# Performance work log

Hardware: AMD Instinct MI355X
Metric: run time of the kernel (lower is better)

Reference implementation:

```python
import jax, jax.numpy as jnp
import numpy as np

N_WAY, N_SHOT, C, H, W = 5, 5, 640, 32, 32
EPS = 1e-12


def conv1x1(x, w, b):
    # 1x1 conv == channel GEMM; w: (C_out, C_in), b: (C_out,)
    return jnp.einsum('bchw,oc->bohw', x, w) + b[None, :, None, None]


def setup_inputs() -> dict:
    key = jax.random.key(0)
    ks = jax.random.split(key, 7)
    B = N_WAY * N_SHOT
    x5 = jax.random.normal(ks[0], (B, C, H, W), jnp.float32)
    Wc = jax.random.normal(ks[1], (C, C), jnp.float32) * 0.02
    bc = jax.random.normal(ks[2], (C,), jnp.float32) * 0.02
    Wq = jax.random.normal(ks[3], (C, C), jnp.float32) * 0.02
    bq = jax.random.normal(ks[4], (C,), jnp.float32) * 0.02
    Wk = jax.random.normal(ks[5], (C, C), jnp.float32) * 0.02
    bk = jax.random.normal(ks[6], (C,), jnp.float32) * 0.02
    return {"x5": x5, "Wc": Wc, "bc": bc, "Wq": Wq, "bq": bq, "Wk": Wk, "bk": bk}


def reference(x5, Wc, bc, Wq, bq, Wk, bk):
    B, Cc, Hh, Ww = x5.shape
    HW = Hh * Ww
    scale = 1.0 / (Cc ** 0.5)

    # residual 1x1 conv, then query_transform applied once (x5 is reassigned)
    x5 = conv1x1(x5, Wc, bc) + x5
    x5 = conv1x1(x5, Wq, bq)

    # query: query_transform applied AGAIN on the already-transformed x5
    xq = conv1x1(x5, Wq, bq).reshape(N_WAY, N_SHOT, Cc, HW)
    xq = xq.transpose(0, 1, 3, 2).reshape(N_WAY, N_SHOT * HW, Cc)
    xk = conv1x1(x5, Wk, bk).reshape(N_WAY, N_SHOT, Cc, HW)
    xk = xk.transpose(0, 2, 1, 3).reshape(N_WAY, Cc, N_SHOT * HW)

    # QK scores per way: (n_way, S*HW, S*HW)
    xw = jnp.matmul(xq, xk) * scale
    # max over key spatial, mean over key shot
    xw = xw.reshape(N_WAY, N_SHOT * HW, N_SHOT, HW).max(-1).mean(-1)
    xw = jax.nn.softmax(xw.reshape(N_WAY, N_SHOT, HW), axis=-1)

    # channel-wise L2 normalize (F.normalize semantics)
    nrm = jnp.maximum(jnp.sqrt((x5 * x5).sum(1, keepdims=True)), EPS)
    norm0 = (x5 / nrm).reshape(N_WAY, N_SHOT, Cc, Hh, Ww)

    # argmax-equality mask over spatial positions
    xw_max = xw.max(-1, keepdims=True)
    mask = (xw == xw_max).astype(x5.dtype).reshape(N_WAY, N_SHOT, 1, Hh, Ww)

    # seeds: masked spatial sum of normalized features -> (n_way, n_shot, C)
    seeds = (norm0 * mask).sum((3, 4))

    # conv3d correlation: out[b,o,h,w] = sum_{k,c} norm0[b,k,c,h,w] * seeds[o,k,c]
    cm = jnp.einsum('bkchw,okc->bohw', norm0, seeds).reshape(N_WAY, N_WAY, HW)
    cmin = cm.min(-1, keepdims=True)
    cmax = cm.max(-1, keepdims=True)
    cm = (cm - cmin) / (cmax - cmin + EPS)
    cormap = cm.reshape(B, 1, Hh, Ww)

    x51 = (x5 * cormap).reshape(N_WAY, N_SHOT, Cc, Hh, Ww)
    proto1 = x51.mean((1, 3, 4))  # (n_way, C)
    return proto1
```

## Files before the change

kernel.cpp:

```cpp
#include <hip/hip_runtime.h>
#include <math.h>

#define NW 5
#define NS 5
#define CDIM 640
#define HWDIM 1024
#define BDIM 25
constexpr int CHW = CDIM * HWDIM;
constexpr int NBIG = BDIM * CHW;
constexpr int WSZ = CDIM * CDIM;
constexpr float QK_SCALE = 0.03952847075210474f;

typedef __attribute__((ext_vector_type(4))) float f32x4;
typedef __attribute__((ext_vector_type(8))) __bf16 bf16x8;
typedef __attribute__((ext_vector_type(4))) __bf16 bf16x4;
typedef __attribute__((ext_vector_type(2))) __bf16 bf16x2;

__device__ __forceinline__ void load_lds16(const __bf16* g, __bf16* l) {
    __builtin_amdgcn_global_load_lds(
        (const __attribute__((address_space(1))) void*)g,
        (__attribute__((address_space(3))) void*)l, 16, 0, 0);
}

__global__ __launch_bounds__(256) void split_f32(const float* __restrict__ s,
                                                 __bf16* __restrict__ dH,
                                                 __bf16* __restrict__ dL, int n4) {
    int i = blockIdx.x * 256 + threadIdx.x;
    if (i >= n4) return;
    f32x4 v = reinterpret_cast<const f32x4*>(s)[i];
    bf16x4 h, lo;
    #pragma unroll
    for (int q = 0; q < 4; ++q) {
        __bf16 hh = (__bf16)v[q];
        h[q] = hh;
        lo[q] = (__bf16)(v[q] - (float)hh);
    }
    reinterpret_cast<bf16x4*>(dH)[i] = h;
    reinterpret_cast<bf16x4*>(dL)[i] = lo;
}

__global__ __launch_bounds__(256) void tsplit(const float* __restrict__ x,
                                              __bf16* __restrict__ dH,
                                              __bf16* __restrict__ dL) {
    __shared__ float sT[32][33];
    const int hw0 = blockIdx.x * 32, c0 = blockIdx.y * 32, b = blockIdx.z;
    const int t = threadIdx.x;
    const int r = t >> 3, q4 = (t & 7) * 4;
    f32x4 v = *reinterpret_cast<const f32x4*>(
        &x[(size_t)b * CHW + (size_t)(c0 + r) * HWDIM + hw0 + q4]);
    #pragma unroll
    for (int i = 0; i < 4; ++i) sT[r][q4 + i] = v[i];
    __syncthreads();
    bf16x4 h, lo;
    #pragma unroll
    for (int i = 0; i < 4; ++i) {
        float xv = sT[q4 + i][r];
        __bf16 hh = (__bf16)xv;
        h[i] = hh;
        lo[i] = (__bf16)(xv - (float)hh);
    }
    size_t off = (size_t)b * CHW + (size_t)(hw0 + r) * CDIM + c0 + q4;
    *reinterpret_cast<bf16x4*>(&dH[off]) = h;
    *reinterpret_cast<bf16x4*>(&dL[off]) = lo;
}


__device__ __forceinline__ void stage_tile(const __bf16* __restrict__ srcH,
                                           const __bf16* __restrict__ srcL,
                                           __bf16* lds, int wv, int l, int c0) {
    const int lch = (l & 7) ^ (l >> 3);
    const int scol = (lch & 3) * 8;
    const int srw = l >> 3;
    const __bf16* src = (lch & 4) ? srcL : srcH;
    #pragma unroll
    for (int i = 0; i < 4; ++i) {
        const int r0 = wv * 32 + i * 8;
        load_lds16(&src[(size_t)(r0 + srw) * CDIM + c0 + scol], &lds[r0 * 64]);
    }
}

template <int RES>
__global__ __launch_bounds__(256) void conv_mfma(
    const __bf16* __restrict__ inH, const __bf16* __restrict__ inL,
    const __bf16* __restrict__ wH, const __bf16* __restrict__ wL,
    const float* __restrict__ bias,
    __bf16* __restrict__ outH, __bf16* __restrict__ outL) {
    __shared__ __bf16 sA[128 * 64];
    __shared__ __bf16 sB[128 * 64];
    const int hw0 = blockIdx.x * 128;
    const int o0 = blockIdx.y * 128;
    const int b = blockIdx.z;
    const int tid = threadIdx.x;
    const int wv = tid >> 6, l = tid & 63;
    const int wo = (wv >> 1) * 64, wh = (wv & 1) * 64;
    const size_t inBase = (size_t)b * CHW;

    const __bf16* wSrcH = wH + (size_t)o0 * CDIM;
    const __bf16* wSrcL = wL + (size_t)o0 * CDIM;
    const __bf16* iSrcH = inH + inBase + (size_t)hw0 * CDIM;
    const __bf16* iSrcL = inL + inBase + (size_t)hw0 * CDIM;

    f32x4 acc[4][4];
    #pragma unroll
    for (int i = 0; i < 4; ++i)
        #pragma unroll
        for (int j = 0; j < 4; ++j) acc[i][j] = (f32x4){0.f, 0.f, 0.f, 0.f};

    const int fr = l & 15, cf = l >> 4;
    const int ehi = (cf ^ (fr & 7)) * 8;

    for (int c0 = 0; c0 < CDIM; c0 += 32) {
        stage_tile(wSrcH, wSrcL, sA, wv, l, c0);
        stage_tile(iSrcH, iSrcL, sB, wv, l, c0);
        __syncthreads();
        bf16x8 aH[4], aL[4], bH[4], bL[4];
        #pragma unroll
        for (int i = 0; i < 4; ++i) {
            const int ra = (wo + i * 16 + fr) * 64;
            const int rb = (wh + i * 16 + fr) * 64;
            aH[i] = *reinterpret_cast<const bf16x8*>(&sA[ra + ehi]);
            aL[i] = *reinterpret_cast<const bf16x8*>(&sA[ra + (ehi ^ 32)]);
            bH[i] = *reinterpret_cast<const bf16x8*>(&sB[rb + ehi]);
            bL[i] = *reinterpret_cast<const bf16x8*>(&sB[rb + (ehi ^ 32)]);
        }
        #pragma unroll
        for (int i = 0; i < 4; ++i)
            #pragma unroll
            for (int j = 0; j < 4; ++j) {
                acc[i][j] = __builtin_amdgcn_mfma_f32_16x16x32_bf16(
                    aH[i], bH[j], acc[i][j], 0, 0, 0);
                acc[i][j] = __builtin_amdgcn_mfma_f32_16x16x32_bf16(
                    aH[i], bL[j], acc[i][j], 0, 0, 0);
                acc[i][j] = __builtin_amdgcn_mfma_f32_16x16x32_bf16(
                    aL[i], bH[j], acc[i][j], 0, 0, 0);
            }
        __syncthreads();
    }

    const int og = (l >> 4) * 4;
    const int cl = l & 15;
    #pragma unroll
    for (int i = 0; i < 4; ++i) {
        const int o = o0 + wo + i * 16 + og;
        const f32x4 bs = *reinterpret_cast<const f32x4*>(&bias[o]);
        #pragma unroll
        for (int j = 0; j < 4; ++j) {
            const int hw = hw0 + wh + j * 16 + cl;
            const size_t off = inBase + (size_t)hw * CDIM + o;
            float r[4];
            #pragma unroll
            for (int q = 0; q < 4; ++q) r[q] = acc[i][j][q] + bs[q];
            if (RES) {
                bf16x4 rh = *reinterpret_cast<const bf16x4*>(&inH[off]);
                bf16x4 rl = *reinterpret_cast<const bf16x4*>(&inL[off]);
                #pragma unroll
                for (int q = 0; q < 4; ++q) r[q] += (float)rh[q] + (float)rl[q];
            }
            bf16x4 oh, ol;
            #pragma unroll
            for (int q = 0; q < 4; ++q) {
                __bf16 hh = (__bf16)r[q];
                oh[q] = hh;
                ol[q] = (__bf16)(r[q] - (float)hh);
            }
            *reinterpret_cast<bf16x4*>(&outH[off]) = oh;
            *reinterpret_cast<bf16x4*>(&outL[off]) = ol;
        }
    }
}

__global__ __launch_bounds__(256) void attn_mfma(
    const __bf16* __restrict__ qH, const __bf16* __restrict__ qL,
    const __bf16* __restrict__ kH, const __bf16* __restrict__ kL,
    float* __restrict__ gpart) {
    __shared__ __bf16 sQ[128 * 64];
    __shared__ __bf16 sK[128 * 64];
    __shared__ float sRed[2][128];
    const int qt = blockIdx.x;
    const int ks = blockIdx.y, wy = blockIdx.z;
    const int sq = qt >> 3, q0 = (qt & 7) * 128;
    const int tid = threadIdx.x;
    const int wv = tid >> 6, l = tid & 63;
    const int wq = (wv >> 1) * 64;
    const int kh = wv & 1;
    const int wk = kh * 64;
    const __bf16* qSrcH = qH + (size_t)(wy * NS + sq) * CHW + (size_t)q0 * CDIM;
    const __bf16* qSrcL = qL + (size_t)(wy * NS + sq) * CHW + (size_t)q0 * CDIM;
    const __bf16* kBaseH = kH + (size_t)(wy * NS + ks) * CHW;
    const __bf16* kBaseL = kL + (size_t)(wy * NS + ks) * CHW;

    float qmax[4][4];
    #pragma unroll
    for (int i = 0; i < 4; ++i)
        #pragma unroll
        for (int q = 0; q < 4; ++q) qmax[i][q] = -INFINITY;

    const int fr = l & 15, cf = l >> 4;
    const int ehi = (cf ^ (fr & 7)) * 8;

    for (int kc = 0; kc < HWDIM; kc += 128) {
        const __bf16* kSrcH = kBaseH + (size_t)kc * CDIM;
        const __bf16* kSrcL = kBaseL + (size_t)kc * CDIM;
        f32x4 acc[4][4];
        #pragma unroll
        for (int i = 0; i < 4; ++i)
            #pragma unroll
            for (int j = 0; j < 4; ++j) acc[i][j] = (f32x4){0.f, 0.f, 0.f, 0.f};

        for (int c0 = 0; c0 < CDIM; c0 += 32) {
            stage_tile(qSrcH, qSrcL, sQ, wv, l, c0);
            stage_tile(kSrcH, kSrcL, sK, wv, l, c0);
            __syncthreads();
            bf16x8 aH[4], aL[4], bH[4], bL[4];
            #pragma unroll
            for (int i = 0; i < 4; ++i) {
                const int ra = (wq + i * 16 + fr) * 64;
                const int rb = (wk + i * 16 + fr) * 64;
                aH[i] = *reinterpret_cast<const bf16x8*>(&sQ[ra + ehi]);
                aL[i] = *reinterpret_cast<const bf16x8*>(&sQ[ra + (ehi ^ 32)]);
                bH[i] = *reinterpret_cast<const bf16x8*>(&sK[rb + ehi]);
                bL[i] = *reinterpret_cast<const bf16x8*>(&sK[rb + (ehi ^ 32)]);
            }
            __builtin_amdgcn_s_setprio(1);
            #pragma unroll
            for (int i = 0; i < 4; ++i)
                #pragma unroll
                for (int j = 0; j < 4; ++j) {
                    acc[i][j] = __builtin_amdgcn_mfma_f32_16x16x32_bf16(
                        aH[i], bH[j], acc[i][j], 0, 0, 0);
                    acc[i][j] = __builtin_amdgcn_mfma_f32_16x16x32_bf16(
                        aH[i], bL[j], acc[i][j], 0, 0, 0);
                    acc[i][j] = __builtin_amdgcn_mfma_f32_16x16x32_bf16(
                        aL[i], bH[j], acc[i][j], 0, 0, 0);
                }
            __builtin_amdgcn_s_setprio(0);
            __syncthreads();
        }
        #pragma unroll
        for (int i = 0; i < 4; ++i)
            #pragma unroll
            for (int q = 0; q < 4; ++q) {
                float m = fmaxf(fmaxf(acc[i][0][q], acc[i][1][q]),
                                fmaxf(acc[i][2][q], acc[i][3][q]));
                qmax[i][q] = fmaxf(qmax[i][q], m);
            }
    }
    #pragma unroll
    for (int i = 0; i < 4; ++i)
        #pragma unroll
        for (int q = 0; q < 4; ++q) {
            float v = qmax[i][q];
            v = fmaxf(v, __shfl_xor(v, 1));
            v = fmaxf(v, __shfl_xor(v, 2));
            v = fmaxf(v, __shfl_xor(v, 4));
            v = fmaxf(v, __shfl_xor(v, 8));
            qmax[i][q] = v;
        }
    if ((l & 15) == 0) {
        const int g = l >> 4;
        #pragma unroll
        for (int i = 0; i < 4; ++i)
            #pragma unroll
            for (int q = 0; q < 4; ++q)
                sRed[kh][wq + i * 16 + g * 4 + q] = qmax[i][q];
    }
    __syncthreads();
    if (tid < 128) {
        float m = fmaxf(sRed[0][tid], sRed[1][tid]);
        gpart[(size_t)(wy * NS + ks) * (NS * HWDIM) + sq * HWDIM + q0 + tid] =
            m * QK_SCALE;
    }
}

__global__ __launch_bounds__(256) void softmax_mask(const float* __restrict__ gpart,
                                                    int* __restrict__ gIdx,
                                                    int* __restrict__ gCnt) {
    const int bb = blockIdx.x;
    const int w = bb / NS, sq = bb % NS;
    const int tid = threadIdx.x;
    __shared__ float sred[256];
    __shared__ int sCnt;

    float v[4];
    #pragma unroll
    for (int i = 0; i < 4; ++i) {
        int hw = tid + 256 * i;
        float s = 0.f;
        #pragma unroll
        for (int ks = 0; ks < NS; ++ks)
            s += gpart[(size_t)(w * NS + ks) * (NS * HWDIM) + sq * HWDIM + hw];
        v[i] = s * 0.2f;
    }
    float m = fmaxf(fmaxf(v[0], v[1]), fmaxf(v[2], v[3]));
    sred[tid] = m;
    __syncthreads();
    for (int s = 128; s > 0; s >>= 1) {
        if (tid < s) sred[tid] = fmaxf(sred[tid], sred[tid + s]);
        __syncthreads();
    }
    float rowmax = sred[0];
    __syncthreads();
    float e[4], ls = 0.f;
    #pragma unroll
    for (int i = 0; i < 4; ++i) { e[i] = expf(v[i] - rowmax); ls += e[i]; }
    sred[tid] = ls;
    __syncthreads();
    for (int s = 128; s > 0; s >>= 1) {
        if (tid < s) sred[tid] += sred[tid + s];
        __syncthreads();
    }
    float ssum = sred[0];
    __syncthreads();
    float p[4], pm = 0.f;
    #pragma unroll
    for (int i = 0; i < 4; ++i) { p[i] = e[i] / ssum; pm = fmaxf(pm, p[i]); }
    sred[tid] = pm;
    __syncthreads();
    for (int s = 128; s > 0; s >>= 1) {
        if (tid < s) sred[tid] = fmaxf(sred[tid], sred[tid + s]);
        __syncthreads();
    }
    float pmax = sred[0];
    if (tid == 0) sCnt = 0;
    __syncthreads();
    #pragma unroll
    for (int i = 0; i < 4; ++i) {
        if (p[i] == pmax) {
            int slot = atomicAdd(&sCnt, 1);
            gIdx[bb * HWDIM + slot] = tid + 256 * i;
        }
    }
    __syncthreads();
    if (tid == 0) gCnt[bb] = sCnt;
}

__global__ __launch_bounds__(256) void nrm_k(const __bf16* __restrict__ yH,
                                             const __bf16* __restrict__ yL,
                                             float* __restrict__ inv) {
    const int row = blockIdx.x * 16 + (threadIdx.x >> 4);
    const int cq = threadIdx.x & 15;
    const size_t base = (size_t)row * CDIM;
    float s = 0.f;
    #pragma unroll
    for (int i = 0; i < 10; ++i) {
        int c = i * 64 + cq * 4;
        bf16x4 h = *reinterpret_cast<const bf16x4*>(&yH[base + c]);
        bf16x4 lo = *reinterpret_cast<const bf16x4*>(&yL[base + c]);
        #pragma unroll
        for (int q = 0; q < 4; ++q) {
            float x = (float)h[q] + (float)lo[q];
            s = fmaf(x, x, s);
        }
    }
    s += __shfl_xor(s, 1);
    s += __shfl_xor(s, 2);
    s += __shfl_xor(s, 4);
    s += __shfl_xor(s, 8);
    if (cq == 0) inv[row] = 1.0f / fmaxf(sqrtf(s), 1e-12f);
}

__global__ __launch_bounds__(640) void seeds_k(const __bf16* __restrict__ yH,
                                               const __bf16* __restrict__ yL,
                                               const float* __restrict__ inv,
                                               const int* __restrict__ gIdx,
                                               const int* __restrict__ gCnt,
                                               float* __restrict__ seeds) {
    const int bb = blockIdx.x, c = threadIdx.x;
    const int cnt = gCnt[bb];
    float s = 0.f;
    for (int e = 0; e < cnt; ++e) {
        int hw = gIdx[bb * HWDIM + e];
        size_t off = (size_t)bb * CHW + (size_t)hw * CDIM + c;
        s += ((float)yH[off] + (float)yL[off]) * inv[bb * HWDIM + hw];
    }
    seeds[bb * CDIM + c] = s;
}

__global__ __launch_bounds__(256) void cm_k(const __bf16* __restrict__ yH,
                                            const __bf16* __restrict__ yL,
                                            const float* __restrict__ inv,
                                            const float* __restrict__ seeds,
                                            float* __restrict__ cm) {
    __shared__ float sS[BDIM * CDIM];
    const int way = blockIdx.y;
    const int tid = threadIdx.x, wv = tid >> 6, l = tid & 63;
    const int hw = blockIdx.x * 4 + wv;
    for (int e = tid; e < BDIM * CDIM; e += 256) sS[e] = seeds[e];
    __syncthreads();
    float acc[NW] = {0.f, 0.f, 0.f, 0.f, 0.f};
    for (int k = 0; k < NS; ++k) {
        const size_t base = (size_t)(way * NS + k) * CHW + (size_t)hw * CDIM;
        float t[NW] = {0.f, 0.f, 0.f, 0.f, 0.f};
        #pragma unroll
        for (int i = 0; i < 5; ++i) {
            int c = (i * 64 + l) * 2;
            bf16x2 h = *reinterpret_cast<const bf16x2*>(&yH[base + c]);
            bf16x2 lo = *reinterpret_cast<const bf16x2*>(&yL[base + c]);
            float x0 = (float)h[0] + (float)lo[0];
            float x1 = (float)h[1] + (float)lo[1];
            #pragma unroll
            for (int o = 0; o < NW; ++o) {
                t[o] = fmaf(x0, sS[(o * NS + k) * CDIM + c], t[o]);
                t[o] = fmaf(x1, sS[(o * NS + k) * CDIM + c + 1], t[o]);
            }
        }
        float iv = inv[(way * NS + k) * HWDIM + hw];
        #pragma unroll
        for (int o = 0; o < NW; ++o) acc[o] = fmaf(t[o], iv, acc[o]);
    }
    #pragma unroll
    for (int o = 0; o < NW; ++o) {
        float v = acc[o];
        v += __shfl_xor(v, 1);
        v += __shfl_xor(v, 2);
        v += __shfl_xor(v, 4);
        v += __shfl_xor(v, 8);
        v += __shfl_xor(v, 16);
        v += __shfl_xor(v, 32);
        if (l == 0) cm[(size_t)(way * NW + o) * HWDIM + hw] = v;
    }
}

__global__ __launch_bounds__(256) void minmax_kernel(float* __restrict__ cm) {
    const int row = blockIdx.x;
    const int tid = threadIdx.x;
    __shared__ float smn[256], smx[256];
    float v[4];
    #pragma unroll
    for (int i = 0; i < 4; ++i) v[i] = cm[(size_t)row * HWDIM + tid + 256 * i];
    float mn = fminf(fminf(v[0], v[1]), fminf(v[2], v[3]));
    float mx = fmaxf(fmaxf(v[0], v[1]), fmaxf(v[2], v[3]));
    smn[tid] = mn;
    smx[tid] = mx;
    __syncthreads();
    for (int s = 128; s > 0; s >>= 1) {
        if (tid < s) {
            smn[tid] = fminf(smn[tid], smn[tid + s]);
            smx[tid] = fmaxf(smx[tid], smx[tid + s]);
        }
        __syncthreads();
    }
    float cmin = smn[0], cmax = smx[0];
    float den = cmax - cmin + 1e-12f;
    #pragma unroll
    for (int i = 0; i < 4; ++i)
        cm[(size_t)row * HWDIM + tid + 256 * i] = (v[i] - cmin) / den;
}

__global__ __launch_bounds__(128) void proto_part_k(const __bf16* __restrict__ yH,
                                                    const __bf16* __restrict__ yL,
                                                    const float* __restrict__ cmn,
                                                    float* __restrict__ part) {
    const int w = blockIdx.x, cc = blockIdx.y, hs = blockIdx.z;
    const int c = cc * 128 + threadIdx.x;
    float s = 0.f;
    for (int i = 0; i < 640; ++i) {
        int g = hs * 640 + i, sh = g >> 10, hw = g & 1023;
        size_t off = (size_t)(w * NS + sh) * CHW + (size_t)hw * CDIM + c;
        s = fmaf((float)yH[off] + (float)yL[off],
                 cmn[(w * NS + sh) * HWDIM + hw], s);
    }
    part[((w * 5 + cc) * 8 + hs) * 128 + threadIdx.x] = s;
}

__global__ __launch_bounds__(128) void proto_red_k(const float* __restrict__ part,
                                                   float* __restrict__ out) {
    const int bid = blockIdx.x;
    float s = 0.f;
    #pragma unroll
    for (int hs = 0; hs < 8; ++hs) s += part[(bid * 8 + hs) * 128 + threadIdx.x];
    const int w = bid / 5, cc = bid % 5;
    out[w * CDIM + cc * 128 + threadIdx.x] = s * (1.0f / 5120.0f);
}

extern "C" void kernel_launch(void* const* d_in, const int* in_sizes, int n_in,
                              void* d_out, int out_size, void* d_ws, size_t ws_size,
                              hipStream_t stream) {
    const float* x5 = (const float*)d_in[0];
    const float* Wc = (const float*)d_in[1];
    const float* bc = (const float*)d_in[2];
    const float* Wq = (const float*)d_in[3];
    const float* bq = (const float*)d_in[4];
    const float* Wk = (const float*)d_in[5];
    const float* bk = (const float*)d_in[6];
    float* out = (float*)d_out;

    __bf16* big = (__bf16*)d_ws;
    __bf16* A_hi = big;
    __bf16* A_lo = big + (size_t)NBIG;
    __bf16* B_hi = big + (size_t)2 * NBIG;
    __bf16* B_lo = big + (size_t)3 * NBIG;
    __bf16* C_hi = big + (size_t)4 * NBIG;
    __bf16* C_lo = big + (size_t)5 * NBIG;
    __bf16* wp = big + (size_t)6 * NBIG;
    __bf16* WcH = wp;
    __bf16* WcL = wp + WSZ;
    __bf16* WqH = wp + 2 * WSZ;
    __bf16* WqL = wp + 3 * WSZ;
    __bf16* WkH = wp + 4 * WSZ;
    __bf16* WkL = wp + 5 * WSZ;
    float* fp = (float*)(wp + 6 * WSZ);
    float* gpart = fp;
    float* invb = fp + 128000;
    float* seedsb = fp + 153600;
    float* cmb = fp + 169600;
    float* partb = fp + 195200;
    int* gIdx = (int*)(fp + 220800);
    int* gCnt = gIdx + BDIM * HWDIM;

    const int W4 = WSZ / 4;
    split_f32<<<dim3((W4 + 255) / 256), 256, 0, stream>>>(Wc, WcH, WcL, W4);
    split_f32<<<dim3((W4 + 255) / 256), 256, 0, stream>>>(Wq, WqH, WqL, W4);
    split_f32<<<dim3((W4 + 255) / 256), 256, 0, stream>>>(Wk, WkH, WkL, W4);
    tsplit<<<dim3(32, 20, 25), 256, 0, stream>>>(x5, A_hi, A_lo);

    dim3 gG(8, 5, 25);
    conv_mfma<1><<<gG, 256, 0, stream>>>(A_hi, A_lo, WcH, WcL, bc, B_hi, B_lo);
    conv_mfma<0><<<gG, 256, 0, stream>>>(B_hi, B_lo, WqH, WqL, bq, C_hi, C_lo);
    conv_mfma<0><<<gG, 256, 0, stream>>>(C_hi, C_lo, WqH, WqL, bq, B_hi, B_lo);
    conv_mfma<0><<<gG, 256, 0, stream>>>(C_hi, C_lo, WkH, WkL, bk, A_hi, A_lo);

    attn_mfma<<<dim3(40, 5, 5), 256, 0, stream>>>(B_hi, B_lo, A_hi, A_lo, gpart);
    softmax_mask<<<25, 256, 0, stream>>>(gpart, gIdx, gCnt);
    nrm_k<<<1600, 256, 0, stream>>>(C_hi, C_lo, invb);
    seeds_k<<<25, 640, 0, stream>>>(C_hi, C_lo, invb, gIdx, gCnt, seedsb);
    cm_k<<<dim3(256, 5), 256, 0, stream>>>(C_hi, C_lo, invb, seedsb, cmb);
    minmax_kernel<<<25, 256, 0, stream>>>(cmb);
    proto_part_k<<<dim3(5, 5, 8), 128, 0, stream>>>(C_hi, C_lo, cmb, partb);
    proto_red_k<<<25, 128, 0, stream>>>(partb, out);
}
```

Before: 1.084 ms.

## Double-buffer LDS tiles in conv and attention MFMA kernels

Both the conv and attention MFMA kernels now use two LDS buffers per operand. The next K-slice is prefetched with global_load_lds while MFMAs run on the current buffer, so global load latency overlaps compute instead of stalling before each step. In the attention kernel the prefetch runs continuously across key-chunk boundaries. LDS per block doubles, which may cut occupancy, and correctness depends on the trailing syncthreads covering the async loads.

```diff
diff --git a/kernel.cpp b/kernel.cpp
--- a/kernel.cpp
+++ b/kernel.cpp
@@ -64,7 +64,6 @@
     *reinterpret_cast<bf16x4*>(&dL[off]) = lo;
 }
 
-
 __device__ __forceinline__ void stage_tile(const __bf16* __restrict__ srcH,
                                            const __bf16* __restrict__ srcL,
                                            __bf16* lds, int wv, int l, int c0) {
@@ -85,8 +84,8 @@
     const __bf16* __restrict__ wH, const __bf16* __restrict__ wL,
     const float* __restrict__ bias,
     __bf16* __restrict__ outH, __bf16* __restrict__ outL) {
-    __shared__ __bf16 sA[128 * 64];
-    __shared__ __bf16 sB[128 * 64];
+    __shared__ __bf16 sA[2][128 * 64];
+    __shared__ __bf16 sB[2][128 * 64];
     const int hw0 = blockIdx.x * 128;
     const int o0 = blockIdx.y * 128;
     const int b = blockIdx.z;
@@ -109,19 +108,26 @@
     const int fr = l & 15, cf = l >> 4;
     const int ehi = (cf ^ (fr & 7)) * 8;
 
-    for (int c0 = 0; c0 < CDIM; c0 += 32) {
-        stage_tile(wSrcH, wSrcL, sA, wv, l, c0);
-        stage_tile(iSrcH, iSrcL, sB, wv, l, c0);
-        __syncthreads();
+    stage_tile(wSrcH, wSrcL, sA[0], wv, l, 0);
+    stage_tile(iSrcH, iSrcL, sB[0], wv, l, 0);
+    __syncthreads();
+
+    constexpr int NT = CDIM / 32;
+    for (int t = 0; t < NT; ++t) {
+        const int cur = t & 1;
+        if (t + 1 < NT) {
+            stage_tile(wSrcH, wSrcL, sA[cur ^ 1], wv, l, (t + 1) * 32);
+            stage_tile(iSrcH, iSrcL, sB[cur ^ 1], wv, l, (t + 1) * 32);
+        }
         bf16x8 aH[4], aL[4], bH[4], bL[4];
         #pragma unroll
         for (int i = 0; i < 4; ++i) {
             const int ra = (wo + i * 16 + fr) * 64;
             const int rb = (wh + i * 16 + fr) * 64;
-            aH[i] = *reinterpret_cast<const bf16x8*>(&sA[ra + ehi]);
-            aL[i] = *reinterpret_cast<const bf16x8*>(&sA[ra + (ehi ^ 32)]);
-            bH[i] = *reinterpret_cast<const bf16x8*>(&sB[rb + ehi]);
-            bL[i] = *reinterpret_cast<const bf16x8*>(&sB[rb + (ehi ^ 32)]);
+            aH[i] = *reinterpret_cast<const bf16x8*>(&sA[cur][ra + ehi]);
+            aL[i] = *reinterpret_cast<const bf16x8*>(&sA[cur][ra + (ehi ^ 32)]);
+            bH[i] = *reinterpret_cast<const bf16x8*>(&sB[cur][rb + ehi]);
+            bL[i] = *reinterpret_cast<const bf16x8*>(&sB[cur][rb + (ehi ^ 32)]);
         }
         #pragma unroll
         for (int i = 0; i < 4; ++i)
@@ -173,8 +179,8 @@
     const __bf16* __restrict__ qH, const __bf16* __restrict__ qL,
     const __bf16* __restrict__ kH, const __bf16* __restrict__ kL,
     float* __restrict__ gpart) {
-    __shared__ __bf16 sQ[128 * 64];
-    __shared__ __bf16 sK[128 * 64];
+    __shared__ __bf16 sQ[2][128 * 64];
+    __shared__ __bf16 sK[2][128 * 64];
     __shared__ float sRed[2][128];
     const int qt = blockIdx.x;
     const int ks = blockIdx.y, wy = blockIdx.z;
@@ -198,28 +204,39 @@
     const int fr = l & 15, cf = l >> 4;
     const int ehi = (cf ^ (fr & 7)) * 8;
 
-    for (int kc = 0; kc < HWDIM; kc += 128) {
-        const __bf16* kSrcH = kBaseH + (size_t)kc * CDIM;
-        const __bf16* kSrcL = kBaseL + (size_t)kc * CDIM;
+    constexpr int NC = CDIM / 32;
+
+    stage_tile(qSrcH, qSrcL, sQ[0], wv, l, 0);
+    stage_tile(kBaseH, kBaseL, sK[0], wv, l, 0);
+    __syncthreads();
+
+    for (int kci = 0; kci < 8; ++kci) {
         f32x4 acc[4][4];
         #pragma unroll
         for (int i = 0; i < 4; ++i)
             #pragma unroll
             for (int j = 0; j < 4; ++j) acc[i][j] = (f32x4){0.f, 0.f, 0.f, 0.f};
 
-        for (int c0 = 0; c0 < CDIM; c0 += 32) {
-            stage_tile(qSrcH, qSrcL, sQ, wv, l, c0);
-            stage_tile(kSrcH, kSrcL, sK, wv, l, c0);
-            __syncthreads();
+        for (int ci = 0; ci < NC; ++ci) {
+            const int step = kci * NC + ci;
+            const int cur = step & 1;
+            int nc = ci + 1, nkc = kci;
+            if (nc == NC) { nc = 0; ++nkc; }
+            if (nkc < 8) {
+                stage_tile(qSrcH, qSrcL, sQ[cur ^ 1], wv, l, nc * 32);
+                stage_tile(kBaseH + (size_t)(nkc * 128) * CDIM,
+                           kBaseL + (size_t)(nkc * 128) * CDIM,
+                           sK[cur ^ 1], wv, l, nc * 32);
+            }
             bf16x8 aH[4], aL[4], bH[4], bL[4];
             #pragma unroll
             for (int i = 0; i < 4; ++i) {
                 const int ra = (wq + i * 16 + fr) * 64;
                 const int rb = (wk + i * 16 + fr) * 64;
-                aH[i] = *reinterpret_cast<const bf16x8*>(&sQ[ra + ehi]);
-                aL[i] = *reinterpret_cast<const bf16x8*>(&sQ[ra + (ehi ^ 32)]);
-                bH[i] = *reinterpret_cast<const bf16x8*>(&sK[rb + ehi]);
-                bL[i] = *reinterpret_cast<const bf16x8*>(&sK[rb + (ehi ^ 32)]);
+                aH[i] = *reinterpret_cast<const bf16x8*>(&sQ[cur][ra + ehi]);
+                aL[i] = *reinterpret_cast<const bf16x8*>(&sQ[cur][ra + (ehi ^ 32)]);
+                bH[i] = *reinterpret_cast<const bf16x8*>(&sK[cur][rb + ehi]);
+                bL[i] = *reinterpret_cast<const bf16x8*>(&sK[cur][rb + (ehi ^ 32)]);
             }
             __builtin_amdgcn_s_setprio(1);
             #pragma unroll
```

Result: no change. 1.082 ms (-0.2%).

## Fold residual conv into Wq, fuse Q/K convs, widen GEMM tiles

Applied to the files above, without the earlier changes.

The residual 1x1 conv followed by the Wq conv is rewritten algebraically as a single GEMM with W2 = Wq·(Wc+I) and bias Wq·bc+bq, both precomputed on device. This removes one full-size conv pass. The two convs that read the same input (Wq and Wk) now run in a single launch with a concatenated bias. Both the conv and attention kernels move to 128x256 tiles to get more reuse per LDS load. In exchange, the weights are rounded differently in the combined product, and the larger accumulator arrays raise register pressure.

```diff
diff --git a/kernel.cpp b/kernel.cpp
--- a/kernel.cpp
+++ b/kernel.cpp
@@ -64,8 +64,43 @@
     *reinterpret_cast<bf16x4*>(&dL[off]) = lo;
 }
 
-
-__device__ __forceinline__ void stage_tile(const __bf16* __restrict__ srcH,
+__global__ __launch_bounds__(256) void wtsplit(const float* __restrict__ W,
+                                               __bf16* __restrict__ dH,
+                                               __bf16* __restrict__ dL) {
+    __shared__ float sT[32][33];
+    const int ci0 = blockIdx.x * 32, t0 = blockIdx.y * 32;
+    const int t = threadIdx.x;
+    const int r = t >> 3, q4 = (t & 7) * 4;
+    f32x4 v = *reinterpret_cast<const f32x4*>(&W[(size_t)(t0 + r) * CDIM + ci0 + q4]);
+    #pragma unroll
+    for (int i = 0; i < 4; ++i) sT[r][q4 + i] = v[i];
+    __syncthreads();
+    bf16x4 h, lo;
+    #pragma unroll
+    for (int i = 0; i < 4; ++i) {
+        float xv = sT[q4 + i][r];
+        if (t0 + q4 + i == ci0 + r) xv += 1.0f;
+        __bf16 hh = (__bf16)xv;
+        h[i] = hh;
+        lo[i] = (__bf16)(xv - (float)hh);
+    }
+    size_t off = (size_t)(ci0 + r) * CDIM + t0 + q4;
+    *reinterpret_cast<bf16x4*>(&dH[off]) = h;
+    *reinterpret_cast<bf16x4*>(&dL[off]) = lo;
+}
+
+__global__ void zero_k(float* __restrict__ p) { p[threadIdx.x] = 0.0f; }
+
+__global__ void bias1_k(const float* __restrict__ Wq, const float* __restrict__ bc,
+                        const float* __restrict__ bq, float* __restrict__ B2) {
+    const int o = threadIdx.x;
+    float s = bq[o];
+    for (int t = 0; t < CDIM; ++t) s = fmaf(Wq[(size_t)o * CDIM + t], bc[t], s);
+    B2[o] = s;
+}
+
+template <int NL>
+__device__ __forceinline__ void stage_rows(const __bf16* __restrict__ srcH,
                                            const __bf16* __restrict__ srcL,
                                            __bf16* lds, int wv, int l, int c0) {
     const int lch = (l & 7) ^ (l >> 3);
@@ -73,14 +108,13 @@
     const int srw = l >> 3;
     const __bf16* src = (lch & 4) ? srcL : srcH;
     #pragma unroll
-    for (int i = 0; i < 4; ++i) {
-        const int r0 = wv * 32 + i * 8;
+    for (int i = 0; i < NL; ++i) {
+        const int r0 = wv * (8 * NL) + i * 8;
         load_lds16(&src[(size_t)(r0 + srw) * CDIM + c0 + scol], &lds[r0 * 64]);
     }
 }
 
-template <int RES>
-__global__ __launch_bounds__(256) void conv_mfma(
+__global__ __launch_bounds__(256) void gemm_sm(
     const __bf16* __restrict__ inH, const __bf16* __restrict__ inL,
     const __bf16* __restrict__ wH, const __bf16* __restrict__ wL,
     const float* __restrict__ bias,
@@ -89,16 +123,14 @@
     __shared__ __bf16 sB[128 * 64];
     const int hw0 = blockIdx.x * 128;
     const int o0 = blockIdx.y * 128;
-    const int b = blockIdx.z;
     const int tid = threadIdx.x;
     const int wv = tid >> 6, l = tid & 63;
     const int wo = (wv >> 1) * 64, wh = (wv & 1) * 64;
-    const size_t inBase = (size_t)b * CHW;
 
     const __bf16* wSrcH = wH + (size_t)o0 * CDIM;
     const __bf16* wSrcL = wL + (size_t)o0 * CDIM;
-    const __bf16* iSrcH = inH + inBase + (size_t)hw0 * CDIM;
-    const __bf16* iSrcL = inL + inBase + (size_t)hw0 * CDIM;
+    const __bf16* iSrcH = inH + (size_t)hw0 * CDIM;
+    const __bf16* iSrcL = inL + (size_t)hw0 * CDIM;
 
     f32x4 acc[4][4];
     #pragma unroll
@@ -110,8 +142,8 @@
     const int ehi = (cf ^ (fr & 7)) * 8;
 
     for (int c0 = 0; c0 < CDIM; c0 += 32) {
-        stage_tile(wSrcH, wSrcL, sA, wv, l, c0);
-        stage_tile(iSrcH, iSrcL, sB, wv, l, c0);
+        stage_rows<4>(wSrcH, wSrcL, sA, wv, l, c0);
+        stage_rows<4>(iSrcH, iSrcL, sB, wv, l, c0);
         __syncthreads();
         bf16x8 aH[4], aL[4], bH[4], bL[4];
         #pragma unroll
@@ -146,22 +178,14 @@
         #pragma unroll
         for (int j = 0; j < 4; ++j) {
             const int hw = hw0 + wh + j * 16 + cl;
-            const size_t off = inBase + (size_t)hw * CDIM + o;
-            float r[4];
-            #pragma unroll
-            for (int q = 0; q < 4; ++q) r[q] = acc[i][j][q] + bs[q];
-            if (RES) {
-                bf16x4 rh = *reinterpret_cast<const bf16x4*>(&inH[off]);
-                bf16x4 rl = *reinterpret_cast<const bf16x4*>(&inL[off]);
-                #pragma unroll
-                for (int q = 0; q < 4; ++q) r[q] += (float)rh[q] + (float)rl[q];
-            }
+            const size_t off = (size_t)hw * CDIM + o;
             bf16x4 oh, ol;
             #pragma unroll
             for (int q = 0; q < 4; ++q) {
-                __bf16 hh = (__bf16)r[q];
+                float r = acc[i][j][q] + bs[q];
+                __bf16 hh = (__bf16)r;
                 oh[q] = hh;
-                ol[q] = (__bf16)(r[q] - (float)hh);
+                ol[q] = (__bf16)(r - (float)hh);
             }
             *reinterpret_cast<bf16x4*>(&outH[off]) = oh;
             *reinterpret_cast<bf16x4*>(&outL[off]) = ol;
@@ -169,12 +193,110 @@
     }
 }
 
-__global__ __launch_bounds__(256) void attn_mfma(
+__global__ __launch_bounds__(256, 2) void conv_big(
+    const __bf16* __restrict__ inH, const __bf16* __restrict__ inL,
+    const __bf16* __restrict__ A0h, const __bf16* __restrict__ A0l,
+    const __bf16* __restrict__ A1h, const __bf16* __restrict__ A1l,
+    const float* __restrict__ bias,
+    __bf16* __restrict__ O0h, __bf16* __restrict__ O0l,
+    __bf16* __restrict__ O1h, __bf16* __restrict__ O1l) {
+    __shared__ __bf16 sA[128 * 64];
+    __shared__ __bf16 sB[256 * 64];
+    const int hw0 = blockIdx.x * 256;
+    const int oy = blockIdx.y;
+    const int seg = oy / 5;
+    const int o0 = (oy % 5) * 128;
+    const int b = blockIdx.z;
+    const int tid = threadIdx.x;
+    const int wv = tid >> 6, l = tid & 63;
+    const int wo = (wv >> 1) * 64;
+    const int wh = (wv & 1) * 128;
+    const size_t inBase = (size_t)b * CHW;
+
+    const __bf16* Ah = seg ? A1h : A0h;
+    const __bf16* Al = seg ? A1l : A0l;
+    __bf16* OhP = seg ? O1h : O0h;
+    __bf16* OlP = seg ? O1l : O0l;
+    const __bf16* aSrcH = Ah + (size_t)o0 * CDIM;
+    const __bf16* aSrcL = Al + (size_t)o0 * CDIM;
+    const __bf16* bSrcH = inH + inBase + (size_t)hw0 * CDIM;
+    const __bf16* bSrcL = inL + inBase + (size_t)hw0 * CDIM;
+
+    f32x4 acc[4][8];
+    #pragma unroll
+    for (int i = 0; i < 4; ++i)
+        #pragma unroll
+        for (int j = 0; j < 8; ++j) acc[i][j] = (f32x4){0.f, 0.f, 0.f, 0.f};
+
+    const int fr = l & 15, cf = l >> 4;
+    const int ehi = (cf ^ (fr & 7)) * 8;
+
+    for (int c0 = 0; c0 < CDIM; c0 += 32) {
+        stage_rows<4>(aSrcH, aSrcL, sA, wv, l, c0);
+        stage_rows<8>(bSrcH, bSrcL, sB, wv, l, c0);
+        __syncthreads();
+        bf16x8 aH[4], aL[4];
+        #pragma unroll
+        for (int i = 0; i < 4; ++i) {
+            const int ra = (wo + i * 16 + fr) * 64;
+            aH[i] = *reinterpret_cast<const bf16x8*>(&sA[ra + ehi]);
+            aL[i] = *reinterpret_cast<const bf16x8*>(&sA[ra + (ehi ^ 32)]);
+        }
+        #pragma unroll
+        for (int jh = 0; jh < 2; ++jh) {
+            bf16x8 bH[4], bL[4];
+            #pragma unroll
+            for (int jj = 0; jj < 4; ++jj) {
+                const int rb = (wh + (jh * 4 + jj) * 16 + fr) * 64;
+                bH[jj] = *reinterpret_cast<const bf16x8*>(&sB[rb + ehi]);
+                bL[jj] = *reinterpret_cast<const bf16x8*>(&sB[rb + (ehi ^ 32)]);
+            }
+            #pragma unroll
+            for (int i = 0; i < 4; ++i)
+                #pragma unroll
+                for (int jj = 0; jj < 4; ++jj) {
+                    const int j = jh * 4 + jj;
+                    acc[i][j] = __builtin_amdgcn_mfma_f32_16x16x32_bf16(
+                        aH[i], bH[jj], acc[i][j], 0, 0, 0);
+                    acc[i][j] = __builtin_amdgcn_mfma_f32_16x16x32_bf16(
+                        aH[i], bL[jj], acc[i][j], 0, 0, 0);
+                    acc[i][j] = __builtin_amdgcn_mfma_f32_16x16x32_bf16(
+                        aL[i], bH[jj], acc[i][j], 0, 0, 0);
+                }
+        }
+        __syncthreads();
+    }
+
+    const int og = (l >> 4) * 4;
+    const int cl = l & 15;
+    #pragma unroll
+    for (int i = 0; i < 4; ++i) {
+        const int oLoc = o0 + wo + i * 16 + og;
+        const f32x4 bs = *reinterpret_cast<const f32x4*>(&bias[oy * 128 + wo + i * 16 + og]);
+        #pragma unroll
+        for (int j = 0; j < 8; ++j) {
+            const int hw = hw0 + wh + j * 16 + cl;
+            const size_t off = inBase + (size_t)hw * CDIM + oLoc;
+            bf16x4 oh, ol;
+            #pragma unroll
+            for (int q = 0; q < 4; ++q) {
+                float r = acc[i][j][q] + bs[q];
+                __bf16 hh = (__bf16)r;
+                oh[q] = hh;
+                ol[q] = (__bf16)(r - (float)hh);
+            }
+            *reinterpret_cast<bf16x4*>(&OhP[off]) = oh;
+            *reinterpret_cast<bf16x4*>(&OlP[off]) = ol;
+        }
+    }
+}
+
+__global__ __launch_bounds__(256, 2) void attn_mfma2(
     const __bf16* __restrict__ qH, const __bf16* __restrict__ qL,
     const __bf16* __restrict__ kH, const __bf16* __restrict__ kL,
     float* __restrict__ gpart) {
     __shared__ __bf16 sQ[128 * 64];
-    __shared__ __bf16 sK[128 * 64];
+    __shared__ __bf16 sK[256 * 64];
     __shared__ float sRed[2][128];
     const int qt = blockIdx.x;
     const int ks = blockIdx.y, wy = blockIdx.z;
@@ -183,7 +305,7 @@
     const int wv = tid >> 6, l = tid & 63;
     const int wq = (wv >> 1) * 64;
     const int kh = wv & 1;
-    const int wk = kh * 64;
+    const int wk = kh * 128;
     const __bf16* qSrcH = qH + (size_t)(wy * NS + sq) * CHW + (size_t)q0 * CDIM;
     const __bf16* qSrcL = qL + (size_t)(wy * NS + sq) * CHW + (size_t)q0 * CDIM;
     const __bf16* kBaseH = kH + (size_t)(wy * NS + ks) * CHW;
@@ -198,41 +320,49 @@
     const int fr = l & 15, cf = l >> 4;
     const int ehi = (cf ^ (fr & 7)) * 8;
 
-    for (int kc = 0; kc < HWDIM; kc += 128) {
-        const __bf16* kSrcH = kBaseH + (size_t)kc * CDIM;
-        const __bf16* kSrcL = kBaseL + (size_t)kc * CDIM;
-        f32x4 acc[4][4];
+    for (int kc = 0; kc < 4; ++kc) {
+        const __bf16* kSrcH = kBaseH + (size_t)(kc * 256) * CDIM;
+        const __bf16* kSrcL = kBaseL + (size_t)(kc * 256) * CDIM;
+        f32x4 acc[4][8];
         #pragma unroll
         for (int i = 0; i < 4; ++i)
             #pragma unroll
-            for (int j = 0; j < 4; ++j) acc[i][j] = (f32x4){0.f, 0.f, 0.f, 0.f};
+            for (int j = 0; j < 8; ++j) acc[i][j] = (f32x4){0.f, 0.f, 0.f, 0.f};
 
         for (int c0 = 0; c0 < CDIM; c0 += 32) {
-            stage_tile(qSrcH, qSrcL, sQ, wv, l, c0);
-            stage_tile(kSrcH, kSrcL, sK, wv, l, c0);
+            stage_rows<4>(qSrcH, qSrcL, sQ, wv, l, c0);
+            stage_rows<8>(kSrcH, kSrcL, sK, wv, l, c0);
             __syncthreads();
-            bf16x8 aH[4], aL[4], bH[4], bL[4];
+            bf16x8 aH[4], aL[4];
             #pragma unroll
             for (int i = 0; i < 4; ++i) {
                 const int ra = (wq + i * 16 + fr) * 64;
-                const int rb = (wk + i * 16 + fr) * 64;
                 aH[i] = *reinterpret_cast<const bf16x8*>(&sQ[ra + ehi]);
                 aL[i] = *reinterpret_cast<const bf16x8*>(&sQ[ra + (ehi ^ 32)]);
-                bH[i] = *reinterpret_cast<const bf16x8*>(&sK[rb + ehi]);
-                bL[i] = *reinterpret_cast<const bf16x8*>(&sK[rb + (ehi ^ 32)]);
             }
             __builtin_amdgcn_s_setprio(1);
             #pragma unroll
-            for (int i = 0; i < 4; ++i)
+            for (int jh = 0; jh < 2; ++jh) {
+                bf16x8 bH[4], bL[4];
                 #pragma unroll
-                for (int j = 0; j < 4; ++j) {
-                    acc[i][j] = __builtin_amdgcn_mfma_f32_16x16x32_bf16(
-                        aH[i], bH[j], acc[i][j], 0, 0, 0);
-                    acc[i][j] = __builtin_amdgcn_mfma_f32_16x16x32_bf16(
-                        aH[i], bL[j], acc[i][j], 0, 0, 0);
-                    acc[i][j] = __builtin_amdgcn_mfma_f32_16x16x32_bf16(
-                        aL[i], bH[j], acc[i][j], 0, 0, 0);
+                for (int jj = 0; jj < 4; ++jj) {
+                    const int rb = (wk + (jh * 4 + jj) * 16 + fr) * 64;
+                    bH[jj] = *reinterpret_cast<const bf16x8*>(&sK[rb + ehi]);
+                    bL[jj] = *reinterpret_cast<const bf16x8*>(&sK[rb + (ehi ^ 32)]);
                 }
+                #pragma unroll
+                for (int i = 0; i < 4; ++i)
+                    #pragma unroll
+                    for (int jj = 0; jj < 4; ++jj) {
+                        const int j = jh * 4 + jj;
+                        acc[i][j] = __builtin_amdgcn_mfma_f32_16x16x32_bf16(
+                            aH[i], bH[jj], acc[i][j], 0, 0, 0);
+                        acc[i][j] = __builtin_amdgcn_mfma_f32_16x16x32_bf16(
+                            aH[i], bL[jj], acc[i][j], 0, 0, 0);
+                        acc[i][j] = __builtin_amdgcn_mfma_f32_16x16x32_bf16(
+                            aL[i], bH[jj], acc[i][j], 0, 0, 0);
+                    }
+            }
             __builtin_amdgcn_s_setprio(0);
             __syncthreads();
         }
@@ -240,8 +370,9 @@
         for (int i = 0; i < 4; ++i)
             #pragma unroll
             for (int q = 0; q < 4; ++q) {
-                float m = fmaxf(fmaxf(acc[i][0][q], acc[i][1][q]),
-                                fmaxf(acc[i][2][q], acc[i][3][q]));
+                float m = acc[i][0][q];
+                #pragma unroll
+                for (int j = 1; j < 8; ++j) m = fmaxf(m, acc[i][j][q]);
                 qmax[i][q] = fmaxf(qmax[i][q], m);
             }
     }
@@ -486,46 +617,57 @@
     float* out = (float*)d_out;
 
     __bf16* big = (__bf16*)d_ws;
-    __bf16* A_hi = big;
-    __bf16* A_lo = big + (size_t)NBIG;
-    __bf16* B_hi = big + (size_t)2 * NBIG;
-    __bf16* B_lo = big + (size_t)3 * NBIG;
-    __bf16* C_hi = big + (size_t)4 * NBIG;
-    __bf16* C_lo = big + (size_t)5 * NBIG;
+    __bf16* Ah = big;
+    __bf16* Al = big + (size_t)NBIG;
+    __bf16* Bh = big + (size_t)2 * NBIG;
+    __bf16* Bl = big + (size_t)3 * NBIG;
+    __bf16* W2H = Bh;
+    __bf16* W2L = Bh + WSZ;
+    __bf16* Ch = big + (size_t)4 * NBIG;
+    __bf16* Cl = big + (size_t)5 * NBIG;
+    __bf16* WcTH = Ch;
+    __bf16* WcTL = Ch + WSZ;
     __bf16* wp = big + (size_t)6 * NBIG;
-    __bf16* WcH = wp;
-    __bf16* WcL = wp + WSZ;
-    __bf16* WqH = wp + 2 * WSZ;
-    __bf16* WqL = wp + 3 * WSZ;
-    __bf16* WkH = wp + 4 * WSZ;
-    __bf16* WkL = wp + 5 * WSZ;
-    float* fp = (float*)(wp + 6 * WSZ);
-    float* gpart = fp;
-    float* invb = fp + 128000;
-    float* seedsb = fp + 153600;
-    float* cmb = fp + 169600;
-    float* partb = fp + 195200;
-    int* gIdx = (int*)(fp + 220800);
+    __bf16* WqH = wp;
+    __bf16* WqL = wp + WSZ;
+    __bf16* WkH = wp + 2 * WSZ;
+    __bf16* WkL = wp + 3 * WSZ;
+    float* fp = (float*)(wp + 4 * WSZ);
+    float* zbias = fp;
+    float* B2 = fp + 640;
+    float* bb2 = fp + 1280;
+    float* gpart = fp + 2560;
+    float* invb = gpart + 128000;
+    float* seedsb = invb + 25600;
+    float* cmb = seedsb + 16000;
+    float* partb = cmb + 25600;
+    int* gIdx = (int*)(partb + 25600);
     int* gCnt = gIdx + BDIM * HWDIM;
 
     const int W4 = WSZ / 4;
-    split_f32<<<dim3((W4 + 255) / 256), 256, 0, stream>>>(Wc, WcH, WcL, W4);
     split_f32<<<dim3((W4 + 255) / 256), 256, 0, stream>>>(Wq, WqH, WqL, W4);
     split_f32<<<dim3((W4 + 255) / 256), 256, 0, stream>>>(Wk, WkH, WkL, W4);
-    tsplit<<<dim3(32, 20, 25), 256, 0, stream>>>(x5, A_hi, A_lo);
-
-    dim3 gG(8, 5, 25);
-    conv_mfma<1><<<gG, 256, 0, stream>>>(A_hi, A_lo, WcH, WcL, bc, B_hi, B_lo);
-    conv_mfma<0><<<gG, 256, 0, stream>>>(B_hi, B_lo, WqH, WqL, bq, C_hi, C_lo);
-    conv_mfma<0><<<gG, 256, 0, stream>>>(C_hi, C_lo, WqH, WqL, bq, B_hi, B_lo);
-    conv_mfma<0><<<gG, 256, 0, stream>>>(C_hi, C_lo, WkH, WkL, bk, A_hi, A_lo);
-
-    attn_mfma<<<dim3(40, 5, 5), 256, 0, stream>>>(B_hi, B_lo, A_hi, A_lo, gpart);
+    wtsplit<<<dim3(20, 20), 256, 0, stream>>>(Wc, WcTH, WcTL);
+    tsplit<<<dim3(32, 20, 25), 256, 0, stream>>>(x5, Ah, Al);
+    zero_k<<<1, 640, 0, stream>>>(zbias);
+    bias1_k<<<1, 640, 0, stream>>>(Wq, bc, bq, B2);
+    hipMemcpyAsync(bb2, bq, CDIM * sizeof(float), hipMemcpyDeviceToDevice, stream);
+    hipMemcpyAsync(bb2 + CDIM, bk, CDIM * sizeof(float), hipMemcpyDeviceToDevice,
+                   stream);
+
+    gemm_sm<<<dim3(5, 5, 1), 256, 0, stream>>>(WqH, WqL, WcTH, WcTL, zbias,
+                                               W2H, W2L);
+    conv_big<<<dim3(4, 5, 25), 256, 0, stream>>>(Ah, Al, W2H, W2L, W2H, W2L,
+                                                 B2, Ch, Cl, Ch, Cl);
+    conv_big<<<dim3(4, 10, 25), 256, 0, stream>>>(Ch, Cl, WqH, WqL, WkH, WkL,
+                                                  bb2, Ah, Al, Bh, Bl);
+
+    attn_mfma2<<<dim3(40, 5, 5), 256, 0, stream>>>(Ah, Al, Bh, Bl, gpart);
     softmax_mask<<<25, 256, 0, stream>>>(gpart, gIdx, gCnt);
-    nrm_k<<<1600, 256, 0, stream>>>(C_hi, C_lo, invb);
-    seeds_k<<<25, 640, 0, stream>>>(C_hi, C_lo, invb, gIdx, gCnt, seedsb);
-    cm_k<<<dim3(256, 5), 256, 0, stream>>>(C_hi, C_lo, invb, seedsb, cmb);
+    nrm_k<<<1600, 256, 0, stream>>>(Ch, Cl, invb);
+    seeds_k<<<25, 640, 0, stream>>>(Ch, Cl, invb, gIdx, gCnt, seedsb);
+    cm_k<<<dim3(256, 5), 256, 0, stream>>>(Ch, Cl, invb, seedsb, cmb);
     minmax_kernel<<<25, 256, 0, stream>>>(cmb);
-    proto_part_k<<<dim3(5, 5, 8), 128, 0, stream>>>(C_hi, C_lo, cmb, partb);
+    proto_part_k<<<dim3(5, 5, 8), 128, 0, stream>>>(Ch, Cl, cmb, partb);
     proto_red_k<<<25, 128, 0, stream>>>(partb, out);
 }
```

Result: faster. 1.007 ms (-7.1%).
